# Kernel tuning notes

Measured on AMD Instinct MI355X. Metric: run time of the kernel, lower is better.

Reference implementation:

```python
import jax, jax.numpy as jnp
import numpy as np

NUM_HEADS = 16


def setup_inputs() -> dict:
    key = jax.random.key(0)
    ks = jax.random.split(key, 9)
    B, N, D = 2, 2048, 1024
    w = 0.02
    return {
        "x": jax.random.normal(ks[0], (B, N, D), dtype=jnp.float32),
        "wq": jax.random.normal(ks[1], (D, D), dtype=jnp.float32) * w,
        "bq": jax.random.normal(ks[2], (D,), dtype=jnp.float32) * w,
        "wk": jax.random.normal(ks[3], (D, D), dtype=jnp.float32) * w,
        "bk": jax.random.normal(ks[4], (D,), dtype=jnp.float32) * w,
        "wv": jax.random.normal(ks[5], (D, D), dtype=jnp.float32) * w,
        "bv": jax.random.normal(ks[6], (D,), dtype=jnp.float32) * w,
        "wo": jax.random.normal(ks[7], (D, D), dtype=jnp.float32) * w,
        "bo": jax.random.normal(ks[8], (D,), dtype=jnp.float32) * w,
    }


def _heads(t, B, N, H, hd):
    # (B, N, D) -> (B, H, N, hd)
    return t.reshape(B, N, H, hd).transpose(0, 2, 1, 3)


def reference(x, wq, bq, wk, bk, wv, bv, wo, bo):
    B, N, D = x.shape
    H = NUM_HEADS
    hd = D // H
    q = _heads(x @ wq.T + bq, B, N, H, hd)
    k = _heads(x @ wk.T + bk, B, N, H, hd)
    v = _heads(x @ wv.T + bv, B, N, H, hd)
    # pairwise L2 distances via GEMM expansion: ||q-k||^2 = |q|^2 + |k|^2 - 2 q.k
    q2 = jnp.sum(q * q, axis=-1)                      # (B, H, N)
    k2 = jnp.sum(k * k, axis=-1)                      # (B, H, N)
    qk = jnp.einsum('bhid,bhjd->bhij', q, k)          # (B, H, N, N)
    d2 = jnp.maximum(q2[..., :, None] + k2[..., None, :] - 2.0 * qk, 1e-12)
    attn = jax.nn.softmax(-jnp.sqrt(d2), axis=-1)     # (B, H, N, N)
    out = jnp.einsum('bhij,bhjd->bhid', attn, v)      # (B, H, N, hd)
    out = out.transpose(0, 2, 1, 3).reshape(B, N, D)
    return out @ wo.T + bo
```

## Files before the change

kernel.cpp:

```cpp
#include <hip/hip_runtime.h>


typedef __attribute__((ext_vector_type(8))) short sh8;
typedef __attribute__((ext_vector_type(4))) short sh4;
typedef __attribute__((ext_vector_type(4))) float f4;

#define QK_SCALE 1.44269504f
#define D2_CLAMP 2.0814e-12f

__device__ __forceinline__ float bf2f(short s) {
  union { unsigned u; float f; } c;
  c.u = ((unsigned)(unsigned short)s) << 16;
  return c.f;
}
__device__ __forceinline__ short f2bf(float f) {
  union { float f; unsigned u; } c;
  c.f = f;
  return (short)((c.u + 0x8000u) >> 16);
}
__device__ __forceinline__ sh8 pack8(f4 a, f4 b) {
  sh8 r;
  r[0] = f2bf(a[0]); r[1] = f2bf(a[1]); r[2] = f2bf(a[2]); r[3] = f2bf(a[3]);
  r[4] = f2bf(b[0]); r[5] = f2bf(b[1]); r[6] = f2bf(b[2]); r[7] = f2bf(b[3]);
  return r;
}
__device__ __forceinline__ float exp2neg(float x) {
  return __builtin_amdgcn_exp2f(-x);
}

#define GLDS16(g, l)                                                      \
  __builtin_amdgcn_global_load_lds(                                       \
      (__attribute__((address_space(1))) void*)(void*)(g),                \
      (__attribute__((address_space(3))) void*)(void*)(l), 16, 0, 0)

__global__ __launch_bounds__(256) void cvt_bf16(const float* __restrict__ src,
                                                short* __restrict__ dst, int n) {
  const int i = (blockIdx.x * 256 + threadIdx.x) * 8;
  if (i < n)
    *(sh8*)(dst + i) = pack8(*(const f4*)(src + i), *(const f4*)(src + i + 4));
}

__global__ __launch_bounds__(256) void cvt_w4(
    const float* __restrict__ wq, const float* __restrict__ wk,
    const float* __restrict__ wv, const float* __restrict__ wo,
    short* __restrict__ dst) {
  const float* srcs[4] = {wq, wk, wv, wo};
  const float* s = srcs[blockIdx.y];
  short* d = dst + (size_t)blockIdx.y * 1048576;
  const int i = (blockIdx.x * 256 + threadIdx.x) * 8;
  *(sh8*)(d + i) = pack8(*(const f4*)(s + i), *(const f4*)(s + i + 4));
}

__global__ __launch_bounds__(256) void gemm_qkvp(
    const float* __restrict__ X, const float* __restrict__ Wq,
    const float* __restrict__ Bq, const float* __restrict__ Wk,
    const float* __restrict__ Bk, const float* __restrict__ Wv,
    const float* __restrict__ Bv, short* __restrict__ Qp,
    short* __restrict__ Kp, short* __restrict__ Vtp, int w0, int nblkP) {
  __shared__ short As[128 * 32];
  __shared__ short Bs[128 * 32];
  const int t = threadIdx.x;
  const int wave = t >> 6;
  const int lane = t & 63;
  const int l15 = lane & 15;
  const int quad = lane >> 4;
  const int m0 = blockIdx.y * 128;
  const int which = blockIdx.x / nblkP;
  const int n0l = (blockIdx.x % nblkP) * 128;
  const int wrow0 = w0 + n0l;
  const float* W = (which == 0) ? Wq : ((which == 1) ? Wk : Wv);
  const float* Bias = (which == 0) ? Bq : ((which == 1) ? Bk : Bv);
  const float qkscl = (which == 2) ? 1.0f : QK_SCALE;
  const int wm = (wave & 1) * 64;
  const int wn = (wave >> 1) * 64;

  f4 acc[4][4];
#pragma unroll
  for (int i = 0; i < 4; ++i)
#pragma unroll
    for (int j = 0; j < 4; ++j) acc[i][j] = (f4){0.f, 0.f, 0.f, 0.f};

  const float* ag = X + (size_t)(m0 + (t >> 2)) * 1024 + (t & 3) * 8;
  const float* bg = W + (size_t)(wrow0 + (t >> 2)) * 1024 + (t & 3) * 8;

  for (int kt = 0; kt < 1024; kt += 32) {
    const sh8 a0 = pack8(*(const f4*)(ag + kt), *(const f4*)(ag + kt + 4));
    const sh8 a1 =
        pack8(*(const f4*)(ag + 65536 + kt), *(const f4*)(ag + 65536 + kt + 4));
    const sh8 b0 = pack8(*(const f4*)(bg + kt), *(const f4*)(bg + kt + 4));
    const sh8 b1 =
        pack8(*(const f4*)(bg + 65536 + kt), *(const f4*)(bg + 65536 + kt + 4));
    __syncthreads();
    *(sh8*)(As + t * 8) = a0;
    *(sh8*)(As + 2048 + t * 8) = a1;
    *(sh8*)(Bs + t * 8) = b0;
    *(sh8*)(Bs + 2048 + t * 8) = b1;
    __syncthreads();
    sh8 af[4], bf[4];
#pragma unroll
    for (int i = 0; i < 4; ++i) {
      af[i] = *(const sh8*)(As + (wm + i * 16 + l15) * 32 + quad * 8);
      bf[i] = *(const sh8*)(Bs + (wn + i * 16 + l15) * 32 + quad * 8);
    }
#pragma unroll
    for (int i = 0; i < 4; ++i)
#pragma unroll
      for (int j = 0; j < 4; ++j)
        acc[i][j] =
            __builtin_amdgcn_mfma_f32_16x16x32_bf16(af[i], bf[j], acc[i][j], 0, 0, 0);
  }

#pragma unroll
  for (int j = 0; j < 4; ++j) {
    const int ngl = n0l + wn + j * 16 + l15;
    const float bias = Bias[w0 + ngl];
    const int hl = ngl >> 6;
    const int d = ngl & 63;
#pragma unroll
    for (int i = 0; i < 4; ++i) {
#pragma unroll
      for (int r = 0; r < 4; ++r) {
        const int m = m0 + wm + i * 16 + quad * 4 + r;
        const int slot = (m >> 11) * 16 + hl;
        const int mm = m & 2047;
        const short o = f2bf((acc[i][j][r] + bias) * qkscl);
        if (which == 0)
          Qp[((size_t)slot * 2048 + mm) * 64 + d] = o;
        else if (which == 1)
          Kp[((size_t)slot * 2048 + mm) * 64 + d] = o;
        else
          Vtp[((size_t)slot * 64 + d) * 2048 + mm] = o;
      }
    }
  }
}

__global__ __launch_bounds__(256) void gemm_qkv_bf(
    const short* __restrict__ X, const short* __restrict__ Wq,
    const float* __restrict__ Bq, const short* __restrict__ Wk,
    const float* __restrict__ Bk, const short* __restrict__ Wv,
    const float* __restrict__ Bv, short* __restrict__ Qp,
    short* __restrict__ Kp, short* __restrict__ Vtp) {
  __shared__ short As[128 * 32];
  __shared__ short Bs[128 * 32];
  const int t = threadIdx.x;
  const int wave = t >> 6;
  const int lane = t & 63;
  const int l15 = lane & 15;
  const int quad = lane >> 4;
  const int m0 = blockIdx.y * 128;
  const int which = blockIdx.x >> 3;
  const int n0l = (blockIdx.x & 7) * 128;
  const short* W = (which == 0) ? Wq : ((which == 1) ? Wk : Wv);
  const float* Bias = (which == 0) ? Bq : ((which == 1) ? Bk : Bv);
  const float qkscl = (which == 2) ? 1.0f : QK_SCALE;
  const int wm = (wave & 1) * 64;
  const int wn = (wave >> 1) * 64;

  f4 acc[4][4];
#pragma unroll
  for (int i = 0; i < 4; ++i)
#pragma unroll
    for (int j = 0; j < 4; ++j) acc[i][j] = (f4){0.f, 0.f, 0.f, 0.f};

  const short* ag = X + (size_t)(m0 + (t >> 2)) * 1024 + (t & 3) * 8;
  const short* bg = W + (size_t)(n0l + (t >> 2)) * 1024 + (t & 3) * 8;
  short* al = As + wave * 512;
  short* bl = Bs + wave * 512;

  for (int kt = 0; kt < 1024; kt += 32) {
    __syncthreads();
    GLDS16(ag + kt, al);
    GLDS16(ag + 65536 + kt, al + 2048);
    GLDS16(bg + kt, bl);
    GLDS16(bg + 65536 + kt, bl + 2048);
    __syncthreads();
    sh8 af[4], bf[4];
#pragma unroll
    for (int i = 0; i < 4; ++i) {
      af[i] = *(const sh8*)(As + (wm + i * 16 + l15) * 32 + quad * 8);
      bf[i] = *(const sh8*)(Bs + (wn + i * 16 + l15) * 32 + quad * 8);
    }
#pragma unroll
    for (int i = 0; i < 4; ++i)
#pragma unroll
      for (int j = 0; j < 4; ++j)
        acc[i][j] =
            __builtin_amdgcn_mfma_f32_16x16x32_bf16(af[i], bf[j], acc[i][j], 0, 0, 0);
  }

#pragma unroll
  for (int j = 0; j < 4; ++j) {
    const int ngl = n0l + wn + j * 16 + l15;
    const float bias = Bias[ngl];
    const int hl = ngl >> 6;
    const int d = ngl & 63;
#pragma unroll
    for (int i = 0; i < 4; ++i) {
#pragma unroll
      for (int r = 0; r < 4; ++r) {
        const int m = m0 + wm + i * 16 + quad * 4 + r;
        const int slot = (m >> 11) * 16 + hl;
        const int mm = m & 2047;
        const short o = f2bf((acc[i][j][r] + bias) * qkscl);
        if (which == 0)
          Qp[((size_t)slot * 2048 + mm) * 64 + d] = o;
        else if (which == 1)
          Kp[((size_t)slot * 2048 + mm) * 64 + d] = o;
        else
          Vtp[((size_t)slot * 64 + d) * 2048 + mm] = o;
      }
    }
  }
}

__global__ __launch_bounds__(256) void sumsq(const short* __restrict__ Qp,
                                             const short* __restrict__ Kp,
                                             float* __restrict__ q2a,
                                             float* __restrict__ k2a, int R) {
  const int tid = blockIdx.x * 256 + threadIdx.x;
  const bool isQ = tid < R;
  const int r = isQ ? tid : tid - R;
  const short* p = (isQ ? Qp : Kp) + (size_t)r * 64;
  float s = 0.f;
#pragma unroll
  for (int i = 0; i < 8; ++i) {
    sh8 v = *(const sh8*)(p + i * 8);
#pragma unroll
    for (int j = 0; j < 8; ++j) {
      float f = bf2f(v[j]);
      s = fmaf(f, f, s);
    }
  }
  (isQ ? q2a : k2a)[r] = s;
}

__global__ __launch_bounds__(256, 2) void attn5(
    const short* __restrict__ Qp, const short* __restrict__ Kp,
    const short* __restrict__ Vtp, const float* __restrict__ q2a,
    const float* __restrict__ k2a, short* __restrict__ attH) {
  __shared__ short Ks[128 * 64];
  __shared__ short Vs[64 * 128];
  const int t = threadIdx.x;
  const int wave = t >> 6;
  const int lane = t & 63;
  const int l15 = lane & 15;
  const int quad = lane >> 4;
  const int id = blockIdx.x;
  const int qt = (id >> 3) & 15;
  const int hb_ = (id & 7) * 4 + (id >> 7);
  const int hy = hb_ & 15;
  const int bz = hb_ >> 4;
  const size_t hb = (size_t)hb_;
  const size_t base = hb * 2048;
  const int qrowA = qt * 128 + wave * 32 + l15;
  const int qrowB = qrowA + 16;

  const short* qpA = Qp + (base + qrowA) * 64 + quad * 8;
  const sh8 qA0 = *(const sh8*)qpA;
  const sh8 qA1 = *(const sh8*)(qpA + 32);
  const short* qpB = Qp + (base + qrowB) * 64 + quad * 8;
  const sh8 qB0 = *(const sh8*)qpB;
  const sh8 qB1 = *(const sh8*)(qpB + 32);
  const float q2A = q2a[base + qrowA];
  const float q2B = q2a[base + qrowB];

  float lA = 0.f, lB = 0.f;
  f4 oA0 = (f4){0.f, 0.f, 0.f, 0.f}, oA1 = oA0, oA2 = oA0, oA3 = oA0;
  f4 oB0 = oA0, oB1 = oA0, oB2 = oA0, oB3 = oA0;

  const float* k2p = k2a + base + quad * 4;

  const int kr = t >> 3, kc = t & 7;
  const int vr = t >> 4, vc = t & 15;
  const short* kg0 = Kp + (base + kr) * 64 + kc * 8;
  const short* vg0 = Vtp + (hb * 64 + vr) * 2048 + vc * 8;
  const int kidx = kr * 64 + ((kc ^ (kr & 7)) * 8);
  const int vidx = vr * 128 + ((vc ^ (vr & 7)) * 8);

  sh8 kp0 = *(const sh8*)kg0;
  sh8 kp1 = *(const sh8*)(kg0 + 32 * 64);
  sh8 kp2 = *(const sh8*)(kg0 + 64 * 64);
  sh8 kp3 = *(const sh8*)(kg0 + 96 * 64);
  sh8 vp0 = *(const sh8*)vg0;
  sh8 vp1 = *(const sh8*)(vg0 + 16 * 2048);
  sh8 vp2 = *(const sh8*)(vg0 + 32 * 2048);
  sh8 vp3 = *(const sh8*)(vg0 + 48 * 2048);

  for (int k0 = 0; k0 < 2048; k0 += 128) {
    __syncthreads();
    *(sh8*)(Ks + kidx) = kp0;
    *(sh8*)(Ks + 32 * 64 + kidx) = kp1;
    *(sh8*)(Ks + 64 * 64 + kidx) = kp2;
    *(sh8*)(Ks + 96 * 64 + kidx) = kp3;
    *(sh8*)(Vs + vidx) = vp0;
    *(sh8*)(Vs + 16 * 128 + vidx) = vp1;
    *(sh8*)(Vs + 32 * 128 + vidx) = vp2;
    *(sh8*)(Vs + 48 * 128 + vidx) = vp3;
    __syncthreads();
    if (k0 + 128 < 2048) {
      const short* kg = kg0 + (size_t)(k0 + 128) * 64;
      kp0 = *(const sh8*)kg;
      kp1 = *(const sh8*)(kg + 32 * 64);
      kp2 = *(const sh8*)(kg + 64 * 64);
      kp3 = *(const sh8*)(kg + 96 * 64);
      const short* vg = vg0 + k0 + 128;
      vp0 = *(const sh8*)vg;
      vp1 = *(const sh8*)(vg + 16 * 2048);
      vp2 = *(const sh8*)(vg + 32 * 2048);
      vp3 = *(const sh8*)(vg + 48 * 2048);
    }

#pragma unroll
    for (int sub = 0; sub < 8; ++sub) {
      const int j = sub * 16;
      const int krow = j + l15;
      const int kcs = (quad ^ (krow & 7)) * 8;
      const sh8 kf0 = *(const sh8*)(Ks + krow * 64 + kcs);
      const sh8 kf1 = *(const sh8*)(Ks + krow * 64 + (kcs ^ 32));
      f4 stA = (f4){0.f, 0.f, 0.f, 0.f};
      f4 stB = (f4){0.f, 0.f, 0.f, 0.f};
      stA = __builtin_amdgcn_mfma_f32_16x16x32_bf16(kf0, qA0, stA, 0, 0, 0);
      stA = __builtin_amdgcn_mfma_f32_16x16x32_bf16(kf1, qA1, stA, 0, 0, 0);
      stB = __builtin_amdgcn_mfma_f32_16x16x32_bf16(kf0, qB0, stB, 0, 0, 0);
      stB = __builtin_amdgcn_mfma_f32_16x16x32_bf16(kf1, qB1, stB, 0, 0, 0);
      const f4 k2v = *(const f4*)(k2p + k0 + j);
      float pA[4], pB[4];
#pragma unroll
      for (int r = 0; r < 4; ++r) {
        const float dA = fmaf(-2.f, stA[r], q2A + k2v[r]);
        pA[r] = exp2neg(__builtin_amdgcn_sqrtf(fabsf(dA)));
        const float dB = fmaf(-2.f, stB[r], q2B + k2v[r]);
        pB[r] = exp2neg(__builtin_amdgcn_sqrtf(fabsf(dB)));
      }
      lA += (pA[0] + pA[1]) + (pA[2] + pA[3]);
      lB += (pB[0] + pB[1]) + (pB[2] + pB[3]);
      sh4 pfA, pfB;
#pragma unroll
      for (int r = 0; r < 4; ++r) {
        pfA[r] = f2bf(pA[r]);
        pfB[r] = f2bf(pB[r]);
      }
      const int vcol = ((sub * 2 + (quad >> 1)) ^ (l15 & 7)) * 8 + (quad & 1) * 4;
      const sh4 vf0 = *(const sh4*)(Vs + l15 * 128 + vcol);
      const sh4 vf1 = *(const sh4*)(Vs + (l15 + 16) * 128 + vcol);
      const sh4 vf2 = *(const sh4*)(Vs + (l15 + 32) * 128 + vcol);
      const sh4 vf3 = *(const sh4*)(Vs + (l15 + 48) * 128 + vcol);
      oA0 = __builtin_amdgcn_mfma_f32_16x16x16bf16_1k(pfA, vf0, oA0, 0, 0, 0);
      oA1 = __builtin_amdgcn_mfma_f32_16x16x16bf16_1k(pfA, vf1, oA1, 0, 0, 0);
      oA2 = __builtin_amdgcn_mfma_f32_16x16x16bf16_1k(pfA, vf2, oA2, 0, 0, 0);
      oA3 = __builtin_amdgcn_mfma_f32_16x16x16bf16_1k(pfA, vf3, oA3, 0, 0, 0);
      oB0 = __builtin_amdgcn_mfma_f32_16x16x16bf16_1k(pfB, vf0, oB0, 0, 0, 0);
      oB1 = __builtin_amdgcn_mfma_f32_16x16x16bf16_1k(pfB, vf1, oB1, 0, 0, 0);
      oB2 = __builtin_amdgcn_mfma_f32_16x16x16bf16_1k(pfB, vf2, oB2, 0, 0, 0);
      oB3 = __builtin_amdgcn_mfma_f32_16x16x16bf16_1k(pfB, vf3, oB3, 0, 0, 0);
    }
  }

  lA += __shfl_xor(lA, 16);
  lA += __shfl_xor(lA, 32);
  lB += __shfl_xor(lB, 16);
  lB += __shfl_xor(lB, 32);
  float ilA[4], ilB[4];
#pragma unroll
  for (int r = 0; r < 4; ++r) {
    ilA[r] = 1.f / __shfl(lA, quad * 4 + r);
    ilB[r] = 1.f / __shfl(lB, quad * 4 + r);
  }

  const int rbA = qt * 128 + wave * 32 + quad * 4;
  const size_t offA = ((size_t)bz * 2048 + rbA) * 1024 + hy * 64 + l15;
  const size_t offB = offA + (size_t)16 * 1024;
  const f4* ocA[4] = {&oA0, &oA1, &oA2, &oA3};
  const f4* ocB[4] = {&oB0, &oB1, &oB2, &oB3};
#pragma unroll
  for (int c = 0; c < 4; ++c)
#pragma unroll
    for (int r = 0; r < 4; ++r) {
      attH[offA + (size_t)r * 1024 + c * 16] = f2bf((*ocA[c])[r] * ilA[r]);
      attH[offB + (size_t)r * 1024 + c * 16] = f2bf((*ocB[c])[r] * ilB[r]);
    }
}

__global__ __launch_bounds__(256) void attn_c(
    const short* __restrict__ Qp, const short* __restrict__ Kp,
    const short* __restrict__ Vtp, const float* __restrict__ q2a,
    const float* __restrict__ k2a, float* __restrict__ attF, int col0) {
  const int t = threadIdx.x;
  const int wave = t >> 6;
  const int lane = t & 63;
  const int l15 = lane & 15;
  const int quad = lane >> 4;
  const int hy = blockIdx.y;
  const int qt = blockIdx.x;
  const size_t base = (size_t)hy * 2048;
  const int qrow = qt * 64 + wave * 16 + l15;

  const short* qp = Qp + (base + qrow) * 64 + quad * 8;
  const sh8 qf0 = *(const sh8*)qp;
  const sh8 qf1 = *(const sh8*)(qp + 32);
  const float q2 = q2a[base + qrow];

  float l_run = 0.f;
  f4 o0 = (f4){0.f, 0.f, 0.f, 0.f}, o1 = o0, o2 = o0, o3 = o0;

  const short* kbase = Kp + (base + l15) * 64 + quad * 8;
  const float* k2p = k2a + base + quad * 4;
  const short* vbase = Vtp + ((size_t)hy * 64 + l15) * 2048 + quad * 4;

  for (int j = 0; j < 2048; j += 16) {
    const sh8 kf0 = *(const sh8*)(kbase + (size_t)j * 64);
    const sh8 kf1 = *(const sh8*)(kbase + (size_t)j * 64 + 32);
    f4 st = (f4){0.f, 0.f, 0.f, 0.f};
    st = __builtin_amdgcn_mfma_f32_16x16x32_bf16(kf0, qf0, st, 0, 0, 0);
    st = __builtin_amdgcn_mfma_f32_16x16x32_bf16(kf1, qf1, st, 0, 0, 0);
    const f4 k2v = *(const f4*)(k2p + j);
    float p[4];
#pragma unroll
    for (int r = 0; r < 4; ++r) {
      const float d2 = fmaxf(fmaf(-2.f, st[r], q2 + k2v[r]), D2_CLAMP);
      p[r] = exp2neg(__builtin_amdgcn_sqrtf(d2));
    }
    l_run += (p[0] + p[1]) + (p[2] + p[3]);
    sh4 pf;
#pragma unroll
    for (int r = 0; r < 4; ++r) pf[r] = f2bf(p[r]);
    const sh4 vf0 = *(const sh4*)(vbase + j);
    const sh4 vf1 = *(const sh4*)(vbase + 16 * 2048 + j);
    const sh4 vf2 = *(const sh4*)(vbase + 32 * 2048 + j);
    const sh4 vf3 = *(const sh4*)(vbase + 48 * 2048 + j);
    o0 = __builtin_amdgcn_mfma_f32_16x16x16bf16_1k(pf, vf0, o0, 0, 0, 0);
    o1 = __builtin_amdgcn_mfma_f32_16x16x16bf16_1k(pf, vf1, o1, 0, 0, 0);
    o2 = __builtin_amdgcn_mfma_f32_16x16x16bf16_1k(pf, vf2, o2, 0, 0, 0);
    o3 = __builtin_amdgcn_mfma_f32_16x16x16bf16_1k(pf, vf3, o3, 0, 0, 0);
  }

  l_run += __shfl_xor(l_run, 16);
  l_run += __shfl_xor(l_run, 32);
  const float il0 = 1.f / __shfl(l_run, quad * 4 + 0);
  const float il1 = 1.f / __shfl(l_run, quad * 4 + 1);
  const float il2 = 1.f / __shfl(l_run, quad * 4 + 2);
  const float il3 = 1.f / __shfl(l_run, quad * 4 + 3);

  const int rowbase = qt * 64 + wave * 16 + quad * 4;
  const f4* oc[4] = {&o0, &o1, &o2, &o3};
  const float il[4] = {il0, il1, il2, il3};
  const size_t off0 = (size_t)rowbase * 1024 + col0 + hy * 64 + l15;
#pragma unroll
  for (int c = 0; c < 4; ++c)
#pragma unroll
    for (int r = 0; r < 4; ++r)
      attF[off0 + (size_t)r * 1024 + c * 16] = (*oc[c])[r] * il[r];
}

__global__ __launch_bounds__(256) void gemm_out_bf64(
    const short* __restrict__ A, const short* __restrict__ W,
    const float* __restrict__ Bias, float* __restrict__ Out) {
  __shared__ short As[64 * 32];
  __shared__ short Bs[128 * 32];
  const int t = threadIdx.x;
  const int wave = t >> 6;
  const int lane = t & 63;
  const int l15 = lane & 15;
  const int quad = lane >> 4;
  const int m0 = blockIdx.y * 64;
  const int n0 = blockIdx.x * 128;
  const int wm = (wave & 1) * 32;
  const int wn = (wave >> 1) * 64;

  f4 acc[2][4];
#pragma unroll
  for (int i = 0; i < 2; ++i)
#pragma unroll
    for (int j = 0; j < 4; ++j) acc[i][j] = (f4){0.f, 0.f, 0.f, 0.f};

  const short* ag = A + (size_t)(m0 + (t >> 2)) * 1024 + (t & 3) * 8;
  const short* bg = W + (size_t)(n0 + (t >> 2)) * 1024 + (t & 3) * 8;
  short* al = As + wave * 512;
  short* bl = Bs + wave * 512;

  for (int kt = 0; kt < 1024; kt += 32) {
    __syncthreads();
    GLDS16(ag + kt, al);
    GLDS16(bg + kt, bl);
    GLDS16(bg + 65536 + kt, bl + 2048);
    __syncthreads();
    sh8 af[2], bf[4];
#pragma unroll
    for (int i = 0; i < 2; ++i)
      af[i] = *(const sh8*)(As + (wm + i * 16 + l15) * 32 + quad * 8);
#pragma unroll
    for (int j = 0; j < 4; ++j)
      bf[j] = *(const sh8*)(Bs + (wn + j * 16 + l15) * 32 + quad * 8);
#pragma unroll
    for (int i = 0; i < 2; ++i)
#pragma unroll
      for (int j = 0; j < 4; ++j)
        acc[i][j] =
            __builtin_amdgcn_mfma_f32_16x16x32_bf16(af[i], bf[j], acc[i][j], 0, 0, 0);
  }

#pragma unroll
  for (int j = 0; j < 4; ++j) {
    const int n = n0 + wn + j * 16 + l15;
    const float bias = Bias[n];
#pragma unroll
    for (int i = 0; i < 2; ++i) {
#pragma unroll
      for (int r = 0; r < 4; ++r) {
        const int m = m0 + wm + i * 16 + quad * 4 + r;
        Out[(size_t)m * 1024 + n] = acc[i][j][r] + bias;
      }
    }
  }
}

__global__ __launch_bounds__(256) void gemm_out_ws64(
    const short* __restrict__ A, const float* __restrict__ W,
    const float* __restrict__ Bias, float* __restrict__ Out) {
  __shared__ short As[64 * 32];
  __shared__ short Bs[128 * 32];
  const int t = threadIdx.x;
  const int wave = t >> 6;
  const int lane = t & 63;
  const int l15 = lane & 15;
  const int quad = lane >> 4;
  const int m0 = blockIdx.y * 64;
  const int n0 = blockIdx.x * 128;
  const int wm = (wave & 1) * 32;
  const int wn = (wave >> 1) * 64;

  f4 acc[2][4];
#pragma unroll
  for (int i = 0; i < 2; ++i)
#pragma unroll
    for (int j = 0; j < 4; ++j) acc[i][j] = (f4){0.f, 0.f, 0.f, 0.f};

  const short* ag = A + (size_t)(m0 + (t >> 2)) * 1024 + (t & 3) * 8;
  const float* bg = W + (size_t)(n0 + (t >> 2)) * 1024 + (t & 3) * 8;
  short* al = As + wave * 512;

  for (int kt = 0; kt < 1024; kt += 32) {
    const sh8 b0 = pack8(*(const f4*)(bg + kt), *(const f4*)(bg + kt + 4));
    const sh8 b1 =
        pack8(*(const f4*)(bg + 65536 + kt), *(const f4*)(bg + 65536 + kt + 4));
    __syncthreads();
    GLDS16(ag + kt, al);
    *(sh8*)(Bs + t * 8) = b0;
    *(sh8*)(Bs + 2048 + t * 8) = b1;
    __syncthreads();
    sh8 af[2], bf[4];
#pragma unroll
    for (int i = 0; i < 2; ++i)
      af[i] = *(const sh8*)(As + (wm + i * 16 + l15) * 32 + quad * 8);
#pragma unroll
    for (int j = 0; j < 4; ++j)
      bf[j] = *(const sh8*)(Bs + (wn + j * 16 + l15) * 32 + quad * 8);
#pragma unroll
    for (int i = 0; i < 2; ++i)
#pragma unroll
      for (int j = 0; j < 4; ++j)
        acc[i][j] =
            __builtin_amdgcn_mfma_f32_16x16x32_bf16(af[i], bf[j], acc[i][j], 0, 0, 0);
  }

#pragma unroll
  for (int j = 0; j < 4; ++j) {
    const int n = n0 + wn + j * 16 + l15;
    const float bias = Bias[n];
#pragma unroll
    for (int i = 0; i < 2; ++i) {
#pragma unroll
      for (int r = 0; r < 4; ++r) {
        const int m = m0 + wm + i * 16 + quad * 4 + r;
        Out[(size_t)m * 1024 + n] = acc[i][j][r] + bias;
      }
    }
  }
}

__global__ __launch_bounds__(256) void outproj_inplace(
    float* __restrict__ AO, const float* __restrict__ W,
    const float* __restrict__ Bias) {
  __shared__ short attS[16 * 264];
  const int t = threadIdx.x;
  const int wave = t >> 6;
  const int lane = t & 63;
  const int l15 = lane & 15;
  const int quad = lane >> 4;
  const int m0 = blockIdx.x * 16;
  const int n0w = wave * 256;

  f4 acc[16];
#pragma unroll
  for (int i = 0; i < 16; ++i) acc[i] = (f4){0.f, 0.f, 0.f, 0.f};

  for (int kc = 0; kc < 4; ++kc) {
    __syncthreads();
#pragma unroll
    for (int i = 0; i < 2; ++i) {
      const int e = i * 2048 + t * 8;
      const int row = e >> 8;
      const int col = e & 255;
      const float* src = AO + (size_t)(m0 + row) * 1024 + kc * 256 + col;
      *(sh8*)(attS + row * 264 + col) =
          pack8(*(const f4*)src, *(const f4*)(src + 4));
    }
    __syncthreads();
    for (int ktl = 0; ktl < 256; ktl += 32) {
      const sh8 af = *(const sh8*)(attS + l15 * 264 + ktl + quad * 8);
      const int kt = kc * 256 + ktl;
#pragma unroll
      for (int nf = 0; nf < 16; ++nf) {
        const float* wp = W + (size_t)(n0w + nf * 16 + l15) * 1024 + kt + quad * 8;
        const sh8 bf = pack8(*(const f4*)wp, *(const f4*)(wp + 4));
        acc[nf] = __builtin_amdgcn_mfma_f32_16x16x32_bf16(af, bf, acc[nf], 0, 0, 0);
      }
    }
  }
  __syncthreads();

#pragma unroll
  for (int nf = 0; nf < 16; ++nf) {
    const int n = n0w + nf * 16 + l15;
    const float bias = Bias[n];
#pragma unroll
    for (int r = 0; r < 4; ++r) {
      const int m = m0 + quad * 4 + r;
      AO[(size_t)m * 1024 + n] = acc[nf][r] + bias;
    }
  }
}

extern "C" void kernel_launch(void* const* d_in, const int* in_sizes, int n_in,
                              void* d_out, int out_size, void* d_ws,
                              size_t ws_size, hipStream_t stream) {
  const float* x = (const float*)d_in[0];
  const float* wq = (const float*)d_in[1];
  const float* bq = (const float*)d_in[2];
  const float* wk = (const float*)d_in[3];
  const float* bk = (const float*)d_in[4];
  const float* wv = (const float*)d_in[5];
  const float* bv = (const float*)d_in[6];
  const float* wo = (const float*)d_in[7];
  const float* bo = (const float*)d_in[8];
  float* out = (float*)d_out;

  const size_t NEED_A2 = 50855936ULL;
  const size_t NEED_A = 34078720ULL;

  if (ws_size >= NEED_A) {
    short* Qp = (short*)d_ws;
    short* Kp = Qp + 4194304;
    short* Vtp = Kp + 4194304;
    short* attAll = Vtp + 4194304;
    float* q2 = (float*)(attAll + 4194304);
    float* k2 = q2 + 65536;

    if (ws_size >= NEED_A2) {
      short* Xb = (short*)(k2 + 65536);
      short* Wqb = Xb + 4194304;
      cvt_bf16<<<2048, 256, 0, stream>>>(x, Xb, 4194304);
      cvt_w4<<<dim3(512, 4), 256, 0, stream>>>(wq, wk, wv, wo, Wqb);
      gemm_qkv_bf<<<dim3(24, 32), 256, 0, stream>>>(
          Xb, Wqb, bq, Wqb + 1048576, bk, Wqb + 2097152, bv, Qp, Kp, Vtp);
      sumsq<<<512, 256, 0, stream>>>(Qp, Kp, q2, k2, 65536);
      attn5<<<512, 256, 0, stream>>>(Qp, Kp, Vtp, q2, k2, attAll);
      gemm_out_bf64<<<dim3(8, 64), 256, 0, stream>>>(attAll, Wqb + 3145728,
                                                     bo, out);
    } else {
      gemm_qkvp<<<dim3(24, 32), 256, 0, stream>>>(x, wq, bq, wk, bk, wv, bv,
                                                  Qp, Kp, Vtp, 0, 8);
      sumsq<<<512, 256, 0, stream>>>(Qp, Kp, q2, k2, 65536);
      attn5<<<512, 256, 0, stream>>>(Qp, Kp, Vtp, q2, k2, attAll);
      gemm_out_ws64<<<dim3(8, 64), 256, 0, stream>>>(attAll, wo, bo, out);
    }
  } else {
    int G = 16;
    while (G > 2 && (size_t)G * 802816ULL > ws_size) G >>= 1;
    short* Qp = (short*)d_ws;
    short* Kp = Qp + (size_t)G * 131072;
    short* Vtp = Kp + (size_t)G * 131072;
    float* q2 = (float*)(Vtp + (size_t)G * 131072);
    float* k2 = q2 + (size_t)G * 2048;

    const int groups = 16 / G;
    for (int b = 0; b < 2; ++b) {
      const float* xb = x + (size_t)b * 2097152;
      float* attB = out + (size_t)b * 2097152;
      for (int g = 0; g < groups; ++g) {
        gemm_qkvp<<<dim3(3 * (G / 2), 16), 256, 0, stream>>>(
            xb, wq, bq, wk, bk, wv, bv, Qp, Kp, Vtp, g * G * 64, G / 2);
        sumsq<<<16 * G, 256, 0, stream>>>(Qp, Kp, q2, k2, G * 2048);
        attn_c<<<dim3(32, G), 256, 0, stream>>>(Qp, Kp, Vtp, q2, k2, attB,
                                                g * G * 64);
      }
    }
    outproj_inplace<<<256, 256, 0, stream>>>(out, wo, bo);
  }
}
```

Before: 227.3 us.

## Split attention key range across two wave groups per block and reduce in LDS

Result: slower. 303.6 us (+33.6%).

```diff
diff --git a/kernel.cpp b/kernel.cpp
--- a/kernel.cpp
+++ b/kernel.cpp
@@ -235,14 +235,16 @@
   (isQ ? q2a : k2a)[r] = s;
 }
 
-__global__ __launch_bounds__(256, 2) void attn5(
+__global__ __launch_bounds__(512, 4) void attn6(
     const short* __restrict__ Qp, const short* __restrict__ Kp,
     const short* __restrict__ Vtp, const float* __restrict__ q2a,
     const float* __restrict__ k2a, short* __restrict__ attH) {
-  __shared__ short Ks[128 * 64];
-  __shared__ short Vs[64 * 128];
+  __shared__ short Ks[2 * 128 * 64];
+  __shared__ short Vs[2 * 64 * 128];
   const int t = threadIdx.x;
   const int wave = t >> 6;
+  const int wg = wave & 3;
+  const int kh = wave >> 2;
   const int lane = t & 63;
   const int l15 = lane & 15;
   const int quad = lane >> 4;
@@ -253,7 +255,7 @@
   const int bz = hb_ >> 4;
   const size_t hb = (size_t)hb_;
   const size_t base = hb * 2048;
-  const int qrowA = qt * 128 + wave * 32 + l15;
+  const int qrowA = qt * 128 + wg * 32 + l15;
   const int qrowB = qrowA + 16;
 
   const short* qpA = Qp + (base + qrowA) * 64 + quad * 8;
@@ -269,12 +271,16 @@
   f4 oA0 = (f4){0.f, 0.f, 0.f, 0.f}, oA1 = oA0, oA2 = oA0, oA3 = oA0;
   f4 oB0 = oA0, oB1 = oA0, oB2 = oA0, oB3 = oA0;
 
-  const float* k2p = k2a + base + quad * 4;
-
-  const int kr = t >> 3, kc = t & 7;
-  const int vr = t >> 4, vc = t & 15;
-  const short* kg0 = Kp + (base + kr) * 64 + kc * 8;
-  const short* vg0 = Vtp + (hb * 64 + vr) * 2048 + vc * 8;
+  const int khk = kh * 1024;
+  const float* k2p = k2a + base + khk + quad * 4;
+
+  const int tl = t & 255;
+  const int kr = tl >> 3, kc = tl & 7;
+  const int vr = tl >> 4, vc = tl & 15;
+  const short* kg0 = Kp + (base + khk + kr) * 64 + kc * 8;
+  const short* vg0 = Vtp + (hb * 64 + vr) * 2048 + khk + vc * 8;
+  short* KsH = Ks + kh * 8192;
+  short* VsH = Vs + kh * 8192;
   const int kidx = kr * 64 + ((kc ^ (kr & 7)) * 8);
   const int vidx = vr * 128 + ((vc ^ (vr & 7)) * 8);
 
@@ -287,18 +293,18 @@
   sh8 vp2 = *(const sh8*)(vg0 + 32 * 2048);
   sh8 vp3 = *(const sh8*)(vg0 + 48 * 2048);
 
-  for (int k0 = 0; k0 < 2048; k0 += 128) {
-    __syncthreads();
-    *(sh8*)(Ks + kidx) = kp0;
-    *(sh8*)(Ks + 32 * 64 + kidx) = kp1;
-    *(sh8*)(Ks + 64 * 64 + kidx) = kp2;
-    *(sh8*)(Ks + 96 * 64 + kidx) = kp3;
-    *(sh8*)(Vs + vidx) = vp0;
-    *(sh8*)(Vs + 16 * 128 + vidx) = vp1;
-    *(sh8*)(Vs + 32 * 128 + vidx) = vp2;
-    *(sh8*)(Vs + 48 * 128 + vidx) = vp3;
-    __syncthreads();
-    if (k0 + 128 < 2048) {
+  for (int k0 = 0; k0 < 1024; k0 += 128) {
+    __syncthreads();
+    *(sh8*)(KsH + kidx) = kp0;
+    *(sh8*)(KsH + 32 * 64 + kidx) = kp1;
+    *(sh8*)(KsH + 64 * 64 + kidx) = kp2;
+    *(sh8*)(KsH + 96 * 64 + kidx) = kp3;
+    *(sh8*)(VsH + vidx) = vp0;
+    *(sh8*)(VsH + 16 * 128 + vidx) = vp1;
+    *(sh8*)(VsH + 32 * 128 + vidx) = vp2;
+    *(sh8*)(VsH + 48 * 128 + vidx) = vp3;
+    __syncthreads();
+    if (k0 + 128 < 1024) {
       const short* kg = kg0 + (size_t)(k0 + 128) * 64;
       kp0 = *(const sh8*)kg;
       kp1 = *(const sh8*)(kg + 32 * 64);
@@ -316,8 +322,8 @@
       const int j = sub * 16;
       const int krow = j + l15;
       const int kcs = (quad ^ (krow & 7)) * 8;
-      const sh8 kf0 = *(const sh8*)(Ks + krow * 64 + kcs);
-      const sh8 kf1 = *(const sh8*)(Ks + krow * 64 + (kcs ^ 32));
+      const sh8 kf0 = *(const sh8*)(KsH + krow * 64 + kcs);
+      const sh8 kf1 = *(const sh8*)(KsH + krow * 64 + (kcs ^ 32));
       f4 stA = (f4){0.f, 0.f, 0.f, 0.f};
       f4 stB = (f4){0.f, 0.f, 0.f, 0.f};
       stA = __builtin_amdgcn_mfma_f32_16x16x32_bf16(kf0, qA0, stA, 0, 0, 0);
@@ -342,10 +348,10 @@
         pfB[r] = f2bf(pB[r]);
       }
       const int vcol = ((sub * 2 + (quad >> 1)) ^ (l15 & 7)) * 8 + (quad & 1) * 4;
-      const sh4 vf0 = *(const sh4*)(Vs + l15 * 128 + vcol);
-      const sh4 vf1 = *(const sh4*)(Vs + (l15 + 16) * 128 + vcol);
-      const sh4 vf2 = *(const sh4*)(Vs + (l15 + 32) * 128 + vcol);
-      const sh4 vf3 = *(const sh4*)(Vs + (l15 + 48) * 128 + vcol);
+      const sh4 vf0 = *(const sh4*)(VsH + l15 * 128 + vcol);
+      const sh4 vf1 = *(const sh4*)(VsH + (l15 + 16) * 128 + vcol);
+      const sh4 vf2 = *(const sh4*)(VsH + (l15 + 32) * 128 + vcol);
+      const sh4 vf3 = *(const sh4*)(VsH + (l15 + 48) * 128 + vcol);
       oA0 = __builtin_amdgcn_mfma_f32_16x16x16bf16_1k(pfA, vf0, oA0, 0, 0, 0);
       oA1 = __builtin_amdgcn_mfma_f32_16x16x16bf16_1k(pfA, vf1, oA1, 0, 0, 0);
       oA2 = __builtin_amdgcn_mfma_f32_16x16x16bf16_1k(pfA, vf2, oA2, 0, 0, 0);
@@ -357,6 +363,36 @@
     }
   }
 
+  __syncthreads();
+  float* oS = (float*)Ks;
+  float* lS = (float*)Vs;
+  const int sl = wg * 64 + lane;
+  if (kh == 1) {
+    *(f4*)(oS + sl * 32 + 0)  = oA0;
+    *(f4*)(oS + sl * 32 + 4)  = oA1;
+    *(f4*)(oS + sl * 32 + 8)  = oA2;
+    *(f4*)(oS + sl * 32 + 12) = oA3;
+    *(f4*)(oS + sl * 32 + 16) = oB0;
+    *(f4*)(oS + sl * 32 + 20) = oB1;
+    *(f4*)(oS + sl * 32 + 24) = oB2;
+    *(f4*)(oS + sl * 32 + 28) = oB3;
+    lS[sl * 2] = lA;
+    lS[sl * 2 + 1] = lB;
+  }
+  __syncthreads();
+  if (kh == 1) return;
+
+  oA0 += *(const f4*)(oS + sl * 32 + 0);
+  oA1 += *(const f4*)(oS + sl * 32 + 4);
+  oA2 += *(const f4*)(oS + sl * 32 + 8);
+  oA3 += *(const f4*)(oS + sl * 32 + 12);
+  oB0 += *(const f4*)(oS + sl * 32 + 16);
+  oB1 += *(const f4*)(oS + sl * 32 + 20);
+  oB2 += *(const f4*)(oS + sl * 32 + 24);
+  oB3 += *(const f4*)(oS + sl * 32 + 28);
+  lA += lS[sl * 2];
+  lB += lS[sl * 2 + 1];
+
   lA += __shfl_xor(lA, 16);
   lA += __shfl_xor(lA, 32);
   lB += __shfl_xor(lB, 16);
@@ -368,7 +404,7 @@
     ilB[r] = 1.f / __shfl(lB, quad * 4 + r);
   }
 
-  const int rbA = qt * 128 + wave * 32 + quad * 4;
+  const int rbA = qt * 128 + wg * 32 + quad * 4;
   const size_t offA = ((size_t)bz * 2048 + rbA) * 1024 + hy * 64 + l15;
   const size_t offB = offA + (size_t)16 * 1024;
   const f4* ocA[4] = {&oA0, &oA1, &oA2, &oA3};
@@ -665,14 +701,14 @@
       gemm_qkv_bf<<<dim3(24, 32), 256, 0, stream>>>(
           Xb, Wqb, bq, Wqb + 1048576, bk, Wqb + 2097152, bv, Qp, Kp, Vtp);
       sumsq<<<512, 256, 0, stream>>>(Qp, Kp, q2, k2, 65536);
-      attn5<<<512, 256, 0, stream>>>(Qp, Kp, Vtp, q2, k2, attAll);
+      attn6<<<512, 512, 0, stream>>>(Qp, Kp, Vtp, q2, k2, attAll);
       gemm_out_bf64<<<dim3(8, 64), 256, 0, stream>>>(attAll, Wqb + 3145728,
                                                      bo, out);
     } else {
       gemm_qkvp<<<dim3(24, 32), 256, 0, stream>>>(x, wq, bq, wk, bk, wv, bv,
                                                   Qp, Kp, Vtp, 0, 8);
       sumsq<<<512, 256, 0, stream>>>(Qp, Kp, q2, k2, 65536);
-      attn5<<<512, 256, 0, stream>>>(Qp, Kp, Vtp, q2, k2, attAll);
+      attn6<<<512, 512, 0, stream>>>(Qp, Kp, Vtp, q2, k2, attAll);
       gemm_out_ws64<<<dim3(8, 64), 256, 0, stream>>>(attAll, wo, bo, out);
     }
   } else {
```
